# Optimization experiments

Measured on AMD Instinct MI355X. Metric: run time of the kernel, lower is better.

## Reference

```python
import jax, jax.numpy as jnp
import numpy as np

N_NODES = 50000
N_EDGES = 500000
HIDDEN = 64
NUM_BASIS = 32
NUM_SH = 4  # (lmax+1)^2 with lmax=1


def _mlp(x, w1, b1, w2, b2):
    # Linear -> SiLU -> Linear, matching nn.Sequential(Linear, SiLU, Linear)
    return jax.nn.silu(x @ w1 + b1) @ w2 + b2


def setup_inputs() -> dict:
    key = jax.random.key(0)
    ks = jax.random.split(key, 10)
    scale_in = 1.0 / np.sqrt(NUM_BASIS)
    scale_h = 1.0 / np.sqrt(HIDDEN)
    return {
        "scalar": jax.random.normal(ks[0], (N_NODES, HIDDEN), dtype=jnp.float32),
        "vector": jax.random.normal(ks[1], (N_NODES, 3, HIDDEN), dtype=jnp.float32),
        "edge_sh": jax.random.normal(ks[2], (N_EDGES, NUM_SH), dtype=jnp.float32),
        "edge_length": jax.random.uniform(ks[3], (N_EDGES, NUM_BASIS), dtype=jnp.float32),
        "edge_index": jax.random.randint(ks[4], (2, N_EDGES), 0, N_NODES, dtype=jnp.int32),
        "sw1": jax.random.normal(ks[5], (NUM_BASIS, HIDDEN), dtype=jnp.float32) * scale_in,
        "sb1": jnp.zeros((HIDDEN,), dtype=jnp.float32),
        "sw2": jax.random.normal(ks[6], (HIDDEN, HIDDEN), dtype=jnp.float32) * scale_h,
        "sb2": jnp.zeros((HIDDEN,), dtype=jnp.float32),
        "vw1": jax.random.normal(ks[7], (NUM_BASIS, HIDDEN), dtype=jnp.float32) * scale_in,
        "vb1": jnp.zeros((HIDDEN,), dtype=jnp.float32),
        "vw2": jax.random.normal(ks[8], (HIDDEN, HIDDEN), dtype=jnp.float32) * scale_h,
        "vb2": jnp.zeros((HIDDEN,), dtype=jnp.float32),
    }


def reference(scalar, vector, edge_sh, edge_length, edge_index,
              sw1, sb1, sw2, sb2, vw1, vb1, vw2, vb2):
    # edge_sh is accepted (as in the torch forward signature) but unused.
    row, col = edge_index[0], edge_index[1]
    n = scalar.shape[0]

    # Edge-wise MLP weights from radial basis expansion: [E, hidden]
    scalar_weights = _mlp(edge_length, sw1, sb1, sw2, sb2)
    # Gather source-node scalars, weight, scatter-add to destination nodes.
    scalar_msg = scalar[col] * scalar_weights                   # [E, hidden]
    out_scalar = jax.ops.segment_sum(scalar_msg, row, num_segments=n)

    vector_weights = _mlp(edge_length, vw1, vb1, vw2, vb2)      # [E, hidden]
    vector_msg = vector[col] * vector_weights[:, None, :]       # [E, 3, hidden]
    out_vector = jax.ops.segment_sum(vector_msg, row, num_segments=n)

    return out_scalar, out_vector
```

## Files before the change

### kernel.cpp

```cpp
#include <hip/hip_runtime.h>

#define HIDDEN 64
#define NB 32
#define SCAN_BLOCK 1024
#define HSTR 72

typedef __attribute__((ext_vector_type(8))) short bf16x8;
typedef __attribute__((ext_vector_type(4))) float f32x4;

static __device__ __forceinline__ unsigned short f2bf(float x) {
    union { float f; unsigned u; } v; v.f = x;
    unsigned r = v.u + 0x7fffu + ((v.u >> 16) & 1u);
    return (unsigned short)(r >> 16);
}
static __device__ __forceinline__ float bf2f(unsigned short s) {
    union { unsigned u; float f; } v; v.u = ((unsigned)s) << 16;
    return v.f;
}

__global__ __launch_bounds__(256) void featpack_kernel(
    const float* __restrict__ scalar,
    const float* __restrict__ vector,
    const int*   __restrict__ edge_index,
    int* __restrict__ counts,
    ushort4* __restrict__ feat,
    int total, int E, int do_feat)
{
    int i = blockIdx.x * 256 + threadIdx.x;
    if (i < E) atomicAdd(&counts[edge_index[i]], 1);
    if (!do_feat || i >= total) return;
    const int n = i >> 6, l = i & 63;
    const float* vp = vector + (size_t)n * 192 + l;
    ushort4 o;
    o.x = f2bf(scalar[i]);
    o.y = f2bf(vp[0]);
    o.z = f2bf(vp[64]);
    o.w = f2bf(vp[128]);
    feat[i] = o;
}

__global__ __launch_bounds__(SCAN_BLOCK) void scan_pass1(
    const int* __restrict__ counts, int* __restrict__ partial,
    int* __restrict__ blocksums, int N)
{
    __shared__ int tmp[SCAN_BLOCK];
    const int t = threadIdx.x;
    const int gid = blockIdx.x * SCAN_BLOCK + t;
    int v = (gid < N) ? counts[gid] : 0;
    tmp[t] = v;
    __syncthreads();
    for (int off = 1; off < SCAN_BLOCK; off <<= 1) {
        int x = (t >= off) ? tmp[t - off] : 0;
        __syncthreads();
        tmp[t] += x;
        __syncthreads();
    }
    if (gid < N) partial[gid] = tmp[t] - v;
    if (t == SCAN_BLOCK - 1) blocksums[blockIdx.x] = tmp[t];
}

__global__ __launch_bounds__(64) void scan_pass2(int* __restrict__ blocksums, int nb)
{
    const int t = threadIdx.x;
    int v = (t < nb) ? blocksums[t] : 0;
    int s = v;
    #pragma unroll
    for (int off = 1; off < 64; off <<= 1) {
        int x = __shfl_up(s, off, 64);
        if (t >= off) s += x;
    }
    if (t < nb) blocksums[t] = s - v;
}

__global__ __launch_bounds__(SCAN_BLOCK) void scan_pass3(
    const int* __restrict__ partial, const int* __restrict__ blocksums,
    int* __restrict__ offsets, int* __restrict__ cursors, int N, int E)
{
    const int gid = blockIdx.x * SCAN_BLOCK + threadIdx.x;
    if (gid < N) {
        int o = partial[gid] + blocksums[blockIdx.x];
        offsets[gid] = o;
        cursors[gid] = o;
    }
    if (blockIdx.x == 0 && threadIdx.x == 0) offsets[N] = E;
}

__global__ __launch_bounds__(256) void scatter_kernel(
    const int* __restrict__ edge_index, int* __restrict__ cursors,
    int* __restrict__ cols, int* __restrict__ eperm, int E)
{
    int i = blockIdx.x * 256 + threadIdx.x;
    if (i < E) {
        int p = atomicAdd(&cursors[edge_index[i]], 1);
        cols[p] = edge_index[E + i];
        eperm[p] = i;
    }
}

__global__ __launch_bounds__(256) void mlp_mfma_kernel(
    const float* __restrict__ edge_length,
    const int*   __restrict__ eperm,
    const float* __restrict__ sw1, const float* __restrict__ sb1,
    const float* __restrict__ sw2, const float* __restrict__ sb2,
    const float* __restrict__ vw1, const float* __restrict__ vb1,
    const float* __restrict__ vw2, const float* __restrict__ vb2,
    unsigned short* __restrict__ W,
    int E, int nchunks)
{
    __shared__ short Hs[4][64 * HSTR];

    const int t    = threadIdx.x;
    const int lane = t & 63;
    const int wid  = t >> 6;
    const int quad = lane >> 4;
    const int l16  = lane & 15;
    short* Hw = Hs[wid];

    const float* w1p[2] = {sw1, vw1};
    const float* b1p[2] = {sb1, vb1};
    const float* w2p[2] = {sw2, vw2};
    const float* b2p[2] = {sb2, vb2};

    bf16x8 w1f[2][4];
    bf16x8 w2f[2][2][4];
    float  b1v[2][4], b2v[2][4];
    #pragma unroll
    for (int m = 0; m < 2; ++m) {
        #pragma unroll
        for (int nt = 0; nt < 4; ++nt) {
            const int col = nt * 16 + l16;
            #pragma unroll
            for (int j = 0; j < 8; ++j)
                w1f[m][nt][j] = (short)f2bf(w1p[m][(quad * 8 + j) * HIDDEN + col]);
            #pragma unroll
            for (int kk = 0; kk < 2; ++kk) {
                #pragma unroll
                for (int j = 0; j < 8; ++j)
                    w2f[m][kk][nt][j] = (short)f2bf(w2p[m][(kk * 32 + quad * 8 + j) * HIDDEN + col]);
            }
            b1v[m][nt] = b1p[m][col];
            b2v[m][nt] = b2p[m][col];
        }
    }

    const int wave_g = blockIdx.x * 4 + wid;
    const int nwaves = gridDim.x * 4;

    for (int c = wave_g; c < nchunks; c += nwaves) {
        const int j0 = c * 64;

        bf16x8 af[4];
        #pragma unroll
        for (int mt = 0; mt < 4; ++mt) {
            int p = j0 + mt * 16 + l16;
            if (p >= E) p = E - 1;
            const int e = eperm[p];
            const float* r = edge_length + (size_t)e * NB + quad * 8;
            float4 u0 = *(const float4*)r;
            float4 u1 = *(const float4*)(r + 4);
            af[mt][0] = (short)f2bf(u0.x); af[mt][1] = (short)f2bf(u0.y);
            af[mt][2] = (short)f2bf(u0.z); af[mt][3] = (short)f2bf(u0.w);
            af[mt][4] = (short)f2bf(u1.x); af[mt][5] = (short)f2bf(u1.y);
            af[mt][6] = (short)f2bf(u1.z); af[mt][7] = (short)f2bf(u1.w);
        }

        #pragma unroll
        for (int m = 0; m < 2; ++m) {
            #pragma unroll
            for (int mt = 0; mt < 4; ++mt) {
                #pragma unroll
                for (int nt = 0; nt < 4; ++nt) {
                    f32x4 cf = {b1v[m][nt], b1v[m][nt], b1v[m][nt], b1v[m][nt]};
                    cf = __builtin_amdgcn_mfma_f32_16x16x32_bf16(af[mt], w1f[m][nt], cf, 0, 0, 0);
                    #pragma unroll
                    for (int r4 = 0; r4 < 4; ++r4) {
                        float x = cf[r4];
                        x = x * __builtin_amdgcn_rcpf(1.0f + __expf(-x));
                        const int row = mt * 16 + quad * 4 + r4;
                        Hw[row * HSTR + nt * 16 + l16] = (short)f2bf(x);
                    }
                }
            }

            #pragma unroll
            for (int mt = 0; mt < 4; ++mt) {
                const int arow = mt * 16 + l16;
                bf16x8 a0 = *(const bf16x8*)(Hw + arow * HSTR + quad * 8);
                bf16x8 a1 = *(const bf16x8*)(Hw + arow * HSTR + 32 + quad * 8);
                #pragma unroll
                for (int nt = 0; nt < 4; ++nt) {
                    f32x4 cf = {b2v[m][nt], b2v[m][nt], b2v[m][nt], b2v[m][nt]};
                    cf = __builtin_amdgcn_mfma_f32_16x16x32_bf16(a1, w2f[m][1][nt], cf, 0, 0, 0);
                    cf = __builtin_amdgcn_mfma_f32_16x16x32_bf16(a0, w2f[m][0][nt], cf, 0, 0, 0);
                    #pragma unroll
                    for (int r4 = 0; r4 < 4; ++r4) {
                        const int row = mt * 16 + quad * 4 + r4;
                        Hw[row * HSTR + nt * 16 + l16] = (short)f2bf(cf[r4]);
                    }
                }
            }

            #pragma unroll
            for (int i = 0; i < 8; ++i) {
                const int row = i * 8 + (lane >> 3);
                bf16x8 v = *(const bf16x8*)(Hw + row * HSTR + (lane & 7) * 8);
                if (j0 + row < E)
                    *(bf16x8*)(W + (size_t)(j0 + row) * 128 + m * 64 + (lane & 7) * 8) = v;
            }
        }
    }
}

__global__ __launch_bounds__(256) void node_kernel_feat(
    const ushort4* __restrict__ feat,
    const int* __restrict__ offsets,
    const int* __restrict__ cols,
    const unsigned short* __restrict__ W,
    float* __restrict__ out_scalar,
    float* __restrict__ out_vector,
    int N)
{
    const int lane = threadIdx.x & 63;
    const int wave = blockIdx.x * 4 + (threadIdx.x >> 6);
    const int nw   = gridDim.x * 4;

    for (int n = wave; n < N; n += nw) {
        const int beg = offsets[n];
        const int end = offsets[n + 1];

        float as = 0.0f, a0 = 0.0f, a1 = 0.0f, a2 = 0.0f;
        float ws = 0, wv = 0, s = 0, v0 = 0, v1 = 0, v2 = 0;

        if (beg < end) {
            const unsigned short* wp = W + (size_t)beg * 128;
            ws = bf2f(wp[lane]); wv = bf2f(wp[64 + lane]);
            const ushort4 f = feat[(size_t)cols[beg] * 64 + lane];
            s = bf2f(f.x); v0 = bf2f(f.y); v1 = bf2f(f.z); v2 = bf2f(f.w);
        }

        for (int j = beg; j < end; ++j) {
            const int jn = (j + 1 < end) ? j + 1 : j;
            const unsigned short* wp = W + (size_t)jn * 128;
            const float wsn = bf2f(wp[lane]);
            const float wvn = bf2f(wp[64 + lane]);
            const ushort4 f = feat[(size_t)cols[jn] * 64 + lane];
            const float sn  = bf2f(f.x);
            const float v0n = bf2f(f.y);
            const float v1n = bf2f(f.z);
            const float v2n = bf2f(f.w);

            as = fmaf(s,  ws, as);
            a0 = fmaf(v0, wv, a0);
            a1 = fmaf(v1, wv, a1);
            a2 = fmaf(v2, wv, a2);

            ws = wsn; wv = wvn; s = sn; v0 = v0n; v1 = v1n; v2 = v2n;
        }

        out_scalar[(size_t)n * HIDDEN + lane] = as;
        float* ov = out_vector + (size_t)n * 3 * HIDDEN;
        ov[lane]       = a0;
        ov[64 + lane]  = a1;
        ov[128 + lane] = a2;
    }
}

__global__ __launch_bounds__(256) void node_kernel_f32(
    const float* __restrict__ scalar,
    const float* __restrict__ vector,
    const int* __restrict__ offsets,
    const int* __restrict__ cols,
    const unsigned short* __restrict__ W,
    float* __restrict__ out_scalar,
    float* __restrict__ out_vector,
    int N)
{
    const int lane = threadIdx.x & 63;
    const int wave = blockIdx.x * 4 + (threadIdx.x >> 6);
    const int nw   = gridDim.x * 4;

    for (int n = wave; n < N; n += nw) {
        const int beg = offsets[n];
        const int end = offsets[n + 1];
        float as = 0.0f, a0 = 0.0f, a1 = 0.0f, a2 = 0.0f;
        for (int j = beg; j < end; ++j) {
            const unsigned short* wp = W + (size_t)j * 128;
            const float w_s = bf2f(wp[lane]);
            const float w_v = bf2f(wp[64 + lane]);
            const int c = cols[j];
            const float* sp = scalar + (size_t)c * HIDDEN;
            const float* vp = vector + (size_t)c * 3 * HIDDEN;
            as = fmaf(sp[lane],       w_s, as);
            a0 = fmaf(vp[lane],       w_v, a0);
            a1 = fmaf(vp[64 + lane],  w_v, a1);
            a2 = fmaf(vp[128 + lane], w_v, a2);
        }
        out_scalar[(size_t)n * HIDDEN + lane] = as;
        float* ov = out_vector + (size_t)n * 3 * HIDDEN;
        ov[lane]       = a0;
        ov[64 + lane]  = a1;
        ov[128 + lane] = a2;
    }
}

extern "C" void kernel_launch(void* const* d_in, const int* in_sizes, int n_in,
                              void* d_out, int out_size, void* d_ws, size_t ws_size,
                              hipStream_t stream) {
    const float* scalar      = (const float*)d_in[0];
    const float* vector      = (const float*)d_in[1];
    const float* edge_length = (const float*)d_in[3];
    const int*   edge_index  = (const int*)d_in[4];
    const float* sw1 = (const float*)d_in[5];
    const float* sb1 = (const float*)d_in[6];
    const float* sw2 = (const float*)d_in[7];
    const float* sb2 = (const float*)d_in[8];
    const float* vw1 = (const float*)d_in[9];
    const float* vb1 = (const float*)d_in[10];
    const float* vw2 = (const float*)d_in[11];
    const float* vb2 = (const float*)d_in[12];

    const int N = in_sizes[0] / HIDDEN;
    const int E = in_sizes[4] / 2;

    float* out_scalar = (float*)d_out;
    float* out_vector = (float*)d_out + (size_t)N * HIDDEN;

    size_t off = 0;
    unsigned short* W = (unsigned short*)d_ws;
    off += (size_t)E * 128 * 2;
    int* cols = (int*)((char*)d_ws + off);
    off += (size_t)E * 4;
    int* eperm = (int*)((char*)d_ws + off);
    off += (size_t)E * 4;
    int* ib = (int*)((char*)d_ws + off);
    int* counts    = ib;
    int* partial   = ib + N;
    int* offsets   = ib + 2 * N;
    int* cursors   = ib + 3 * N + 1;
    int* blocksums = ib + 4 * N + 1;
    off += ((size_t)4 * N + 1 + 64) * 4;
    off = (off + 15) & ~(size_t)15;
    ushort4* feat = (ushort4*)((char*)d_ws + off);
    const bool use_feat = (off + (size_t)N * 64 * 8) <= ws_size;

    hipMemsetAsync(counts, 0, (size_t)N * sizeof(int), stream);

    const int egrid = (E + 255) / 256;

    {
        const int total = N * 64;
        int cover = total > E ? total : E;
        featpack_kernel<<<(cover + 255) / 256, 256, 0, stream>>>(
            scalar, vector, edge_index, counts, feat, total, E, use_feat ? 1 : 0);
    }

    const int nb = (N + SCAN_BLOCK - 1) / SCAN_BLOCK;
    scan_pass1<<<nb, SCAN_BLOCK, 0, stream>>>(counts, partial, blocksums, N);
    scan_pass2<<<1, 64, 0, stream>>>(blocksums, nb);
    scan_pass3<<<nb, SCAN_BLOCK, 0, stream>>>(partial, blocksums, offsets, cursors, N, E);
    scatter_kernel<<<egrid, 256, 0, stream>>>(edge_index, cursors, cols, eperm, E);

    const int nchunks = (E + 63) / 64;
    mlp_mfma_kernel<<<1024, 256, 0, stream>>>(
        edge_length, eperm,
        sw1, sb1, sw2, sb2, vw1, vb1, vw2, vb2,
        W, E, nchunks);

    const int ngrid = (N + 3) / 4;
    if (use_feat) {
        node_kernel_feat<<<ngrid, 256, 0, stream>>>(
            feat, offsets, cols, W, out_scalar, out_vector, N);
    } else {
        node_kernel_f32<<<ngrid, 256, 0, stream>>>(
            scalar, vector, offsets, cols, W, out_scalar, out_vector, N);
    }
}
```

Baseline: 349.4 us.

## Fuse CSR build into one cooperative kernel and deepen node-loop prefetch

The memset, count/featpack, three scan passes and scatter kernel are merged into a single cooperative kernel launched with 256 blocks. Phases are separated by grid.sync, and the scan is done as per-block scans plus a one-block scan of the block sums. This removes several launches and kernel boundaries, but runs the feature packing and atomics on a smaller grid-stride grid and adds grid-wide barriers. It also assumes N fits within 256×256 entries. Separately, the node gather loop now keeps four edges of loads in flight instead of one, to hide gather latency at the cost of more registers.

```diff
diff --git a/kernel.cpp b/kernel.cpp
--- a/kernel.cpp
+++ b/kernel.cpp
@@ -1,9 +1,13 @@
 #include <hip/hip_runtime.h>
+#include <hip/hip_cooperative_groups.h>
+
+namespace cg = cooperative_groups;
 
 #define HIDDEN 64
 #define NB 32
-#define SCAN_BLOCK 1024
 #define HSTR 72
+#define PRE_BLOCKS 256
+#define PRE_THREADS 256
 
 typedef __attribute__((ext_vector_type(8))) short bf16x8;
 typedef __attribute__((ext_vector_type(4))) float f32x4;
@@ -18,79 +22,82 @@
     return v.f;
 }
 
-__global__ __launch_bounds__(256) void featpack_kernel(
+__global__ __launch_bounds__(PRE_THREADS) void prep_kernel(
     const float* __restrict__ scalar,
     const float* __restrict__ vector,
     const int*   __restrict__ edge_index,
     int* __restrict__ counts,
     ushort4* __restrict__ feat,
-    int total, int E, int do_feat)
+    int* __restrict__ offsets,
+    int* __restrict__ cursors,
+    int* __restrict__ blocksums,
+    int* __restrict__ cols,
+    int* __restrict__ eperm,
+    int N, int E, int total, int do_feat)
 {
-    int i = blockIdx.x * 256 + threadIdx.x;
-    if (i < E) atomicAdd(&counts[edge_index[i]], 1);
-    if (!do_feat || i >= total) return;
-    const int n = i >> 6, l = i & 63;
-    const float* vp = vector + (size_t)n * 192 + l;
-    ushort4 o;
-    o.x = f2bf(scalar[i]);
-    o.y = f2bf(vp[0]);
-    o.z = f2bf(vp[64]);
-    o.w = f2bf(vp[128]);
-    feat[i] = o;
-}
-
-__global__ __launch_bounds__(SCAN_BLOCK) void scan_pass1(
-    const int* __restrict__ counts, int* __restrict__ partial,
-    int* __restrict__ blocksums, int N)
-{
-    __shared__ int tmp[SCAN_BLOCK];
-    const int t = threadIdx.x;
-    const int gid = blockIdx.x * SCAN_BLOCK + t;
-    int v = (gid < N) ? counts[gid] : 0;
+    cg::grid_group grid = cg::this_grid();
+    __shared__ int tmp[PRE_THREADS];
+
+    const int t   = threadIdx.x;
+    const int gid = blockIdx.x * PRE_THREADS + t;
+    const int nth = gridDim.x * PRE_THREADS;
+
+    for (int i = gid; i < N; i += nth) counts[i] = 0;
+    grid.sync();
+
+    for (int i = gid; i < E; i += nth)
+        atomicAdd(&counts[edge_index[i]], 1);
+    if (do_feat) {
+        for (int i = gid; i < total; i += nth) {
+            const int n = i >> 6, l = i & 63;
+            const float* vp = vector + (size_t)n * 192 + l;
+            ushort4 o;
+            o.x = f2bf(scalar[i]);
+            o.y = f2bf(vp[0]);
+            o.z = f2bf(vp[64]);
+            o.w = f2bf(vp[128]);
+            feat[i] = o;
+        }
+    }
+    grid.sync();
+
+    const int base = blockIdx.x * PRE_THREADS;
+    int v = (base + t < N) ? counts[base + t] : 0;
     tmp[t] = v;
     __syncthreads();
-    for (int off = 1; off < SCAN_BLOCK; off <<= 1) {
+    for (int off = 1; off < PRE_THREADS; off <<= 1) {
         int x = (t >= off) ? tmp[t - off] : 0;
         __syncthreads();
         tmp[t] += x;
         __syncthreads();
     }
-    if (gid < N) partial[gid] = tmp[t] - v;
-    if (t == SCAN_BLOCK - 1) blocksums[blockIdx.x] = tmp[t];
-}
-
-__global__ __launch_bounds__(64) void scan_pass2(int* __restrict__ blocksums, int nb)
-{
-    const int t = threadIdx.x;
-    int v = (t < nb) ? blocksums[t] : 0;
-    int s = v;
-    #pragma unroll
-    for (int off = 1; off < 64; off <<= 1) {
-        int x = __shfl_up(s, off, 64);
-        if (t >= off) s += x;
-    }
-    if (t < nb) blocksums[t] = s - v;
-}
-
-__global__ __launch_bounds__(SCAN_BLOCK) void scan_pass3(
-    const int* __restrict__ partial, const int* __restrict__ blocksums,
-    int* __restrict__ offsets, int* __restrict__ cursors, int N, int E)
-{
-    const int gid = blockIdx.x * SCAN_BLOCK + threadIdx.x;
-    if (gid < N) {
-        int o = partial[gid] + blocksums[blockIdx.x];
-        offsets[gid] = o;
-        cursors[gid] = o;
-    }
-    if (blockIdx.x == 0 && threadIdx.x == 0) offsets[N] = E;
-}
-
-__global__ __launch_bounds__(256) void scatter_kernel(
-    const int* __restrict__ edge_index, int* __restrict__ cursors,
-    int* __restrict__ cols, int* __restrict__ eperm, int E)
-{
-    int i = blockIdx.x * 256 + threadIdx.x;
-    if (i < E) {
+    const int excl = tmp[t] - v;
+    if (t == PRE_THREADS - 1) blocksums[blockIdx.x] = tmp[t];
+    grid.sync();
+
+    if (blockIdx.x == 0) {
+        int b = blocksums[t];
+        tmp[t] = b;
+        __syncthreads();
+        for (int off = 1; off < PRE_THREADS; off <<= 1) {
+            int x = (t >= off) ? tmp[t - off] : 0;
+            __syncthreads();
+            tmp[t] += x;
+            __syncthreads();
+        }
+        blocksums[t] = tmp[t] - b;
+    }
+    grid.sync();
+
+    if (base + t < N) {
+        const int o = excl + blocksums[blockIdx.x];
+        offsets[base + t] = o;
+        cursors[base + t] = o;
+    }
+    if (gid == 0) offsets[N] = E;
+    grid.sync();
+
+    for (int i = gid; i < E; i += nth) {
         int p = atomicAdd(&cursors[edge_index[i]], 1);
         cols[p] = edge_index[E + i];
         eperm[p] = i;
@@ -229,32 +236,50 @@
         const int end = offsets[n + 1];
 
         float as = 0.0f, a0 = 0.0f, a1 = 0.0f, a2 = 0.0f;
-        float ws = 0, wv = 0, s = 0, v0 = 0, v1 = 0, v2 = 0;
 
         if (beg < end) {
-            const unsigned short* wp = W + (size_t)beg * 128;
-            ws = bf2f(wp[lane]); wv = bf2f(wp[64 + lane]);
-            const ushort4 f = feat[(size_t)cols[beg] * 64 + lane];
-            s = bf2f(f.x); v0 = bf2f(f.y); v1 = bf2f(f.z); v2 = bf2f(f.w);
-        }
-
-        for (int j = beg; j < end; ++j) {
-            const int jn = (j + 1 < end) ? j + 1 : j;
-            const unsigned short* wp = W + (size_t)jn * 128;
-            const float wsn = bf2f(wp[lane]);
-            const float wvn = bf2f(wp[64 + lane]);
-            const ushort4 f = feat[(size_t)cols[jn] * 64 + lane];
-            const float sn  = bf2f(f.x);
-            const float v0n = bf2f(f.y);
-            const float v1n = bf2f(f.z);
-            const float v2n = bf2f(f.w);
-
-            as = fmaf(s,  ws, as);
-            a0 = fmaf(v0, wv, a0);
-            a1 = fmaf(v1, wv, a1);
-            a2 = fmaf(v2, wv, a2);
-
-            ws = wsn; wv = wvn; s = sn; v0 = v0n; v1 = v1n; v2 = v2n;
+            float wsA, wvA, sA, v0A, v1A, v2A;
+            float wsB, wvB, sB, v0B, v1B, v2B;
+            float wsC, wvC, sC, v0C, v1C, v2C;
+            float wsD, wvD, sD, v0D, v1D, v2D;
+
+#define LOADX(WS, WV, S, V0, V1, V2, jj) {                                   \
+            const int _ok = (jj) < end;                                       \
+            const int _j  = _ok ? (jj) : (end - 1);                           \
+            const unsigned short* _wp = W + (size_t)_j * 128;                 \
+            WS = _ok ? bf2f(_wp[lane]) : 0.0f;                                \
+            WV = _ok ? bf2f(_wp[64 + lane]) : 0.0f;                           \
+            const ushort4 _f = feat[(size_t)cols[_j] * 64 + lane];            \
+            S = bf2f(_f.x); V0 = bf2f(_f.y); V1 = bf2f(_f.z); V2 = bf2f(_f.w); }
+
+#define CONSX(WS, WV, S, V0, V1, V2) {                                        \
+            as = fmaf(S,  WS, as);                                            \
+            a0 = fmaf(V0, WV, a0);                                            \
+            a1 = fmaf(V1, WV, a1);                                            \
+            a2 = fmaf(V2, WV, a2); }
+
+            LOADX(wsA, wvA, sA, v0A, v1A, v2A, beg);
+            LOADX(wsB, wvB, sB, v0B, v1B, v2B, beg + 1);
+            LOADX(wsC, wvC, sC, v0C, v1C, v2C, beg + 2);
+            LOADX(wsD, wvD, sD, v0D, v1D, v2D, beg + 3);
+
+            int j = beg;
+            for (; j + 4 < end; j += 4) {
+                CONSX(wsA, wvA, sA, v0A, v1A, v2A);
+                LOADX(wsA, wvA, sA, v0A, v1A, v2A, j + 4);
+                CONSX(wsB, wvB, sB, v0B, v1B, v2B);
+                LOADX(wsB, wvB, sB, v0B, v1B, v2B, j + 5);
+                CONSX(wsC, wvC, sC, v0C, v1C, v2C);
+                LOADX(wsC, wvC, sC, v0C, v1C, v2C, j + 6);
+                CONSX(wsD, wvD, sD, v0D, v1D, v2D);
+                LOADX(wsD, wvD, sD, v0D, v1D, v2D, j + 7);
+            }
+            CONSX(wsA, wvA, sA, v0A, v1A, v2A);
+            CONSX(wsB, wvB, sB, v0B, v1B, v2B);
+            CONSX(wsC, wvC, sC, v0C, v1C, v2C);
+            CONSX(wsD, wvD, sD, v0D, v1D, v2D);
+#undef LOADX
+#undef CONSX
         }
 
         out_scalar[(size_t)n * HIDDEN + lane] = as;
@@ -334,31 +359,27 @@
     off += (size_t)E * 4;
     int* ib = (int*)((char*)d_ws + off);
     int* counts    = ib;
-    int* partial   = ib + N;
-    int* offsets   = ib + 2 * N;
-    int* cursors   = ib + 3 * N + 1;
-    int* blocksums = ib + 4 * N + 1;
-    off += ((size_t)4 * N + 1 + 64) * 4;
+    int* offsets   = ib + N;
+    int* cursors   = ib + 2 * N + 1;
+    int* blocksums = ib + 3 * N + 1;
+    off += ((size_t)3 * N + 1 + PRE_BLOCKS) * 4;
     off = (off + 15) & ~(size_t)15;
     ushort4* feat = (ushort4*)((char*)d_ws + off);
     const bool use_feat = (off + (size_t)N * 64 * 8) <= ws_size;
 
-    hipMemsetAsync(counts, 0, (size_t)N * sizeof(int), stream);
-
-    const int egrid = (E + 255) / 256;
-
     {
-        const int total = N * 64;
-        int cover = total > E ? total : E;
-        featpack_kernel<<<(cover + 255) / 256, 256, 0, stream>>>(
-            scalar, vector, edge_index, counts, feat, total, E, use_feat ? 1 : 0);
-    }
-
-    const int nb = (N + SCAN_BLOCK - 1) / SCAN_BLOCK;
-    scan_pass1<<<nb, SCAN_BLOCK, 0, stream>>>(counts, partial, blocksums, N);
-    scan_pass2<<<1, 64, 0, stream>>>(blocksums, nb);
-    scan_pass3<<<nb, SCAN_BLOCK, 0, stream>>>(partial, blocksums, offsets, cursors, N, E);
-    scatter_kernel<<<egrid, 256, 0, stream>>>(edge_index, cursors, cols, eperm, E);
+        int total   = N * 64;
+        int do_feat = use_feat ? 1 : 0;
+        void* args[] = {
+            (void*)&scalar, (void*)&vector, (void*)&edge_index,
+            (void*)&counts, (void*)&feat, (void*)&offsets, (void*)&cursors,
+            (void*)&blocksums, (void*)&cols, (void*)&eperm,
+            (void*)&N, (void*)&E, (void*)&total, (void*)&do_feat
+        };
+        hipLaunchCooperativeKernel((void*)prep_kernel,
+                                   dim3(PRE_BLOCKS), dim3(PRE_THREADS),
+                                   args, 0, stream);
+    }
 
     const int nchunks = (E + 63) / 64;
     mlp_mfma_kernel<<<1024, 256, 0, stream>>>(
```

New measurement: 519.3 us. 1.49x slower.
